# Kernel optimization log

Hardware: AMD Instinct MI355X
Metric: run time of the kernel (lower is better)

The kernel has to match this reference:

```python
import jax, jax.numpy as jnp
import numpy as np

B, S, HID = 2, 2048, 4096
NH, NKV, HD = 32, 8, 128
N_REP = NH // NKV
SCALING = HD ** -0.5


def rotate_half(x):
    x1, x2 = x[..., : x.shape[-1] // 2], x[..., x.shape[-1] // 2 :]
    return jnp.concatenate((-x2, x1), axis=-1)


def setup_inputs() -> dict:
    key = jax.random.key(0)
    ks = jax.random.split(key, 8)
    hidden_states = jax.random.normal(ks[0], (B, S, HID), dtype=jnp.float32)
    # rotary embeddings (realistic cos/sin from inverse-frequency angles)
    inv_freq = 1.0 / (10000.0 ** (jnp.arange(0, HD, 2, dtype=jnp.float32) / HD))
    pos = jnp.arange(S, dtype=jnp.float32)
    ang = pos[:, None] * inv_freq[None, :]  # [S, HD/2]
    emb = jnp.concatenate([ang, ang], axis=-1)  # [S, HD]
    cos = jnp.broadcast_to(jnp.cos(emb)[None], (B, S, HD))
    sin = jnp.broadcast_to(jnp.sin(emb)[None], (B, S, HD))
    # additive causal mask [B,1,S,S]
    causal = jnp.triu(jnp.full((S, S), -1e9, dtype=jnp.float32), k=1)
    attention_mask = jnp.broadcast_to(causal[None, None], (B, 1, S, S))
    std = HID ** -0.5
    Wq = jax.random.normal(ks[1], (NH * HD, HID), dtype=jnp.float32) * std
    Wk = jax.random.normal(ks[2], (NKV * HD, HID), dtype=jnp.float32) * std
    Wv = jax.random.normal(ks[3], (NKV * HD, HID), dtype=jnp.float32) * std
    Wo = jax.random.normal(ks[4], (HID, NH * HD), dtype=jnp.float32) * std
    return {"hidden_states": hidden_states, "cos": cos, "sin": sin,
            "attention_mask": attention_mask, "Wq": Wq, "Wk": Wk, "Wv": Wv, "Wo": Wo}


def reference(hidden_states, cos, sin, attention_mask, Wq, Wk, Wv, Wo):
    b, s, _ = hidden_states.shape
    # projections (nn.Linear: x @ W.T), reshape to [B, H, S, D]
    q = (hidden_states @ Wq.T).reshape(b, s, NH, HD).transpose(0, 2, 1, 3)
    k = (hidden_states @ Wk.T).reshape(b, s, NKV, HD).transpose(0, 2, 1, 3)
    v = (hidden_states @ Wv.T).reshape(b, s, NKV, HD).transpose(0, 2, 1, 3)
    # RoPE, cos/sin broadcast over head dim
    c, sn = cos[:, None], sin[:, None]  # [B,1,S,D]
    q = q * c + rotate_half(q) * sn
    k = k * c + rotate_half(k) * sn
    # GQA repeat_kv
    k = jnp.repeat(k, N_REP, axis=1)
    v = jnp.repeat(v, N_REP, axis=1)
    # eager attention
    attn = jnp.einsum("bhqd,bhkd->bhqk", q, k) * SCALING
    attn = attn + attention_mask[:, :, :, : k.shape[2]]
    attn = jax.nn.softmax(attn.astype(jnp.float32), axis=-1).astype(q.dtype)
    out = jnp.einsum("bhqk,bhkd->bhqd", attn, v)
    out = out.transpose(0, 2, 1, 3).reshape(b, s, NH * HD)
    return out @ Wo.T
```

## Files before the change

kernel.cpp:

```cpp
#include <hip/hip_runtime.h>


typedef __bf16 bf16x8 __attribute__((ext_vector_type(8)));
typedef __bf16 bf16x4 __attribute__((ext_vector_type(4)));
typedef float floatx4 __attribute__((ext_vector_type(4)));

#define S_LEN 2048
#define HIDN  4096
#define NH    32
#define NKV   8
#define HD    128

__device__ inline void async_copy16(const void* g, void* l) {
  __builtin_amdgcn_global_load_lds(
      (const __attribute__((address_space(1))) void*)g,
      (__attribute__((address_space(3))) void*)l, 16, 0, 0);
}

template<int N> __device__ __forceinline__ void waitv() {
  static_assert(N == 0 || N == 6 || N == 8, "vmcnt");
  if constexpr (N == 0)      asm volatile("s_waitcnt vmcnt(0)" ::: "memory");
  else if constexpr (N == 6) asm volatile("s_waitcnt vmcnt(6)" ::: "memory");
  else                       asm volatile("s_waitcnt vmcnt(8)" ::: "memory");
}

__global__ __launch_bounds__(256) void cvt_bf16(const float* __restrict__ src,
                                                __bf16* __restrict__ dst, int n8)
{
  int i = blockIdx.x * 256 + threadIdx.x;
  if (i >= n8) return;
  const float4* s = (const float4*)src + (size_t)i * 2;
  float4 a = s[0], b = s[1];
  bf16x8 r = {(__bf16)a.x, (__bf16)a.y, (__bf16)a.z, (__bf16)a.w,
              (__bf16)b.x, (__bf16)b.y, (__bf16)b.z, (__bf16)b.w};
  *((bf16x8*)dst + i) = r;
}

__device__ __forceinline__ void gemm_core64(
    const __bf16* __restrict__ A, const __bf16* __restrict__ WB,
    __bf16* lds, int m0, int n0, int tid, floatx4 (&acc)[4][4])
{
  constexpr int A_BYTES = 128 * 64 * 2;
  constexpr int STAGE_B = (128 + 256) * 64 * 2;

  const int wave = tid >> 6, lane = tid & 63;
  const int quad = lane >> 4, l16 = lane & 15;
  const int wm = wave >> 2, wn = wave & 3;

  int a_off[2], b_off[4];
  #pragma unroll
  for (int ra = 0; ra < 2; ra++) {
    int idx = ra * 512 + tid;
    int row = idx >> 3, chunk = (idx & 7) ^ (row & 7);
    a_off[ra] = (m0 + row) * HIDN + chunk * 8;
  }
  #pragma unroll
  for (int rb = 0; rb < 4; rb++) {
    int idx = rb * 512 + tid;
    int row = idx >> 3, chunk = (idx & 7) ^ (row & 7);
    b_off[rb] = (n0 + row) * HIDN + chunk * 8;
  }

  const int swq  = (quad ^ (l16 & 3)) * 16;
  const int kxor = ((l16 >> 2) & 1) * 64;
  const int a_rd = (wm * 64 + l16) * 128 + swq;
  const int b_rd = A_BYTES + (wn * 64 + l16) * 128 + swq;

  #pragma unroll
  for (int mi = 0; mi < 4; mi++)
    #pragma unroll
    for (int ni = 0; ni < 4; ni++) acc[mi][ni] = (floatx4){0.f, 0.f, 0.f, 0.f};

  char* ldsb = (char*)lds;
  auto stage = [&](int kt, int slotB) {
    char* sb = ldsb + slotB;
    const size_t ko = (size_t)kt * 64;
    #pragma unroll
    for (int ra = 0; ra < 2; ra++)
      async_copy16(A + ko + a_off[ra], sb + (ra * 512 + tid) * 16);
    #pragma unroll
    for (int rb = 0; rb < 4; rb++)
      async_copy16(WB + ko + b_off[rb], sb + A_BYTES + (rb * 512 + tid) * 16);
  };
  auto read_frags = [&](int slotB, bf16x8 (&av)[4][2], bf16x8 (&bv)[4][2]) {
    const char* sb = ldsb + slotB;
    #pragma unroll
    for (int kk = 0; kk < 2; kk++) {
      const int kb = (kk << 6) ^ kxor;
      #pragma unroll
      for (int ni = 0; ni < 4; ni++)
        bv[ni][kk] = *(const bf16x8*)(sb + b_rd + ni * 2048 + kb);
      #pragma unroll
      for (int mi = 0; mi < 4; mi++)
        av[mi][kk] = *(const bf16x8*)(sb + a_rd + mi * 2048 + kb);
    }
  };
  auto mfma_tile = [&](bf16x8 (&av)[4][2], bf16x8 (&bv)[4][2]) {
    __builtin_amdgcn_s_setprio(1);
    #pragma unroll
    for (int kk = 0; kk < 2; kk++)
      #pragma unroll
      for (int mi = 0; mi < 4; mi++)
        #pragma unroll
        for (int ni = 0; ni < 4; ni++)
          acc[mi][ni] = __builtin_amdgcn_mfma_f32_16x16x32_bf16(
              bv[ni][kk], av[mi][kk], acc[mi][ni], 0, 0, 0);
    __builtin_amdgcn_s_setprio(0);
  };

  bf16x8 avA[4][2], bvA[4][2], avB[4][2], bvB[4][2];

  stage(0, 0);
  stage(1, STAGE_B);
  waitv<6>();
  __builtin_amdgcn_s_barrier();
  asm volatile("" ::: "memory");
  read_frags(0, avA, bvA);

  int oRead = STAGE_B, oStage = 2 * STAGE_B, oFree = 0;

#define GBODY(KT, AVc, BVc, AVn, BVn)                          \
  {                                                            \
    stage((KT) + 2, oStage);                                   \
    waitv<6>();                                                \
    asm volatile("s_waitcnt lgkmcnt(0)" ::: "memory");         \
    __builtin_amdgcn_s_barrier();                              \
    asm volatile("" ::: "memory");                             \
    read_frags(oRead, AVn, BVn);                               \
    mfma_tile(AVc, BVc);                                       \
    int t_ = oFree; oFree = oRead; oRead = oStage; oStage = t_;\
  }

  for (int kt = 0; kt < 62; kt += 2) {
    GBODY(kt,     avA, bvA, avB, bvB);
    GBODY(kt + 1, avB, bvB, avA, bvA);
  }
  {
    waitv<0>();
    asm volatile("s_waitcnt lgkmcnt(0)" ::: "memory");
    __builtin_amdgcn_s_barrier();
    asm volatile("" ::: "memory");
    read_frags(oRead, avB, bvB);
    mfma_tile(avA, bvA);
  }
  mfma_tile(avB, bvB);
#undef GBODY
}

__global__ __launch_bounds__(512, 2) void qkv_gemm_bf16(
    const __bf16* __restrict__ A, const __bf16* __restrict__ WB,
    __bf16* __restrict__ Qb, __bf16* __restrict__ Kb, __bf16* __restrict__ Vt)
{
  __shared__ __bf16 lds[3 * (128 + 256) * 32 * 2];
  const int tid = threadIdx.x;
  const int m0 = blockIdx.y * 128, n0 = blockIdx.x * 256;
  floatx4 acc[4][4];
  gemm_core64(A, WB, lds, m0, n0, tid, acc);

  const int wave = tid >> 6, lane = tid & 63;
  const int quad = lane >> 4, l16 = lane & 15;
  const int wm = wave >> 2, wn = wave & 3;
  #pragma unroll
  for (int mi = 0; mi < 4; mi++) {
    int m = m0 + wm * 64 + mi * 16 + l16;
    int b = m >> 11, s = m & (S_LEN - 1);
    #pragma unroll
    for (int ni = 0; ni < 4; ni++) {
      int nb = n0 + wn * 64 + ni * 16 + quad * 4;
      if (nb < 4096) {
        int hh = nb >> 7, d = nb & 127;
        bf16x4 v = {(__bf16)acc[mi][ni][0], (__bf16)acc[mi][ni][1],
                    (__bf16)acc[mi][ni][2], (__bf16)acc[mi][ni][3]};
        *(bf16x4*)&Qb[(((size_t)b * NH + hh) * S_LEN + s) * HD + d] = v;
      } else if (nb < 5120) {
        int nl = nb - 4096, hh = nl >> 7, d = nl & 127;
        bf16x4 v = {(__bf16)acc[mi][ni][0], (__bf16)acc[mi][ni][1],
                    (__bf16)acc[mi][ni][2], (__bf16)acc[mi][ni][3]};
        *(bf16x4*)&Kb[(((size_t)b * NKV + hh) * S_LEN + s) * HD + d] = v;
      } else {
        int nl = nb - 5120, hh = nl >> 7, d = nl & 127;
        #pragma unroll
        for (int r = 0; r < 4; r++)
          Vt[(((size_t)b * NKV + hh) * HD + d + r) * S_LEN + s] =
              (__bf16)acc[mi][ni][r];
      }
    }
  }
}

__global__ __launch_bounds__(512, 2) void out_gemm_bf16(
    const __bf16* __restrict__ A, const __bf16* __restrict__ WB,
    float* __restrict__ C)
{
  __shared__ __bf16 lds[3 * (128 + 256) * 32 * 2];
  const int tid = threadIdx.x;
  const int m0 = blockIdx.y * 128, n0 = blockIdx.x * 256;
  floatx4 acc[4][4];
  gemm_core64(A, WB, lds, m0, n0, tid, acc);

  const int wave = tid >> 6, lane = tid & 63;
  const int quad = lane >> 4, l16 = lane & 15;
  const int wm = wave >> 2, wn = wave & 3;
  #pragma unroll
  for (int mi = 0; mi < 4; mi++) {
    int m = m0 + wm * 64 + mi * 16 + l16;
    #pragma unroll
    for (int ni = 0; ni < 4; ni++) {
      int nb = n0 + wn * 64 + ni * 16 + quad * 4;
      *(floatx4*)&C[(size_t)m * HIDN + nb] = acc[mi][ni];
    }
  }
}

__global__ __launch_bounds__(256) void qkv_gemm_f32(
    const float* __restrict__ A, const float* __restrict__ Wq,
    const float* __restrict__ Wk, const float* __restrict__ Wv,
    __bf16* __restrict__ Qb, __bf16* __restrict__ Kb, __bf16* __restrict__ Vt)
{
  __shared__ __bf16 As[128 * 40];
  __shared__ __bf16 Bs[128 * 40];
  const int tid  = threadIdx.x;
  const int wave = tid >> 6, lane = tid & 63;
  const int quad = lane >> 4, l16 = lane & 15;
  const int wrow = (wave >> 1) * 64, wcol = (wave & 1) * 64;
  const int m0 = blockIdx.y * 128;
  const int n0 = blockIdx.x * 128;

  const float* W; int wr0; int sel;
  if (n0 < 4096)      { W = Wq; wr0 = n0;        sel = 0; }
  else if (n0 < 5120) { W = Wk; wr0 = n0 - 4096; sel = 1; }
  else                { W = Wv; wr0 = n0 - 5120; sel = 2; }

  floatx4 acc[4][4];
  #pragma unroll
  for (int i = 0; i < 4; i++)
    #pragma unroll
    for (int j = 0; j < 4; j++) acc[i][j] = (floatx4){0.f, 0.f, 0.f, 0.f};

  for (int k0 = 0; k0 < HIDN; k0 += 32) {
    __syncthreads();
    #pragma unroll
    for (int it = 0; it < 4; ++it) {
      int c = tid + it * 256;
      int row = c >> 3, c4 = (c & 7) * 4;
      float4 va = *(const float4*)(A + (size_t)(m0 + row) * HIDN + k0 + c4);
      __bf16* da = &As[row * 40 + c4];
      da[0] = (__bf16)va.x; da[1] = (__bf16)va.y; da[2] = (__bf16)va.z; da[3] = (__bf16)va.w;
      float4 vb = *(const float4*)(W + (size_t)(wr0 + row) * HIDN + k0 + c4);
      __bf16* db = &Bs[row * 40 + c4];
      db[0] = (__bf16)vb.x; db[1] = (__bf16)vb.y; db[2] = (__bf16)vb.z; db[3] = (__bf16)vb.w;
    }
    __syncthreads();
    bf16x8 af[4], bfr[4];
    #pragma unroll
    for (int i = 0; i < 4; i++)
      af[i] = *(const bf16x8*)&As[(wrow + i * 16 + l16) * 40 + quad * 8];
    #pragma unroll
    for (int j = 0; j < 4; j++)
      bfr[j] = *(const bf16x8*)&Bs[(wcol + j * 16 + l16) * 40 + quad * 8];
    #pragma unroll
    for (int i = 0; i < 4; i++)
      #pragma unroll
      for (int j = 0; j < 4; j++)
        acc[i][j] = __builtin_amdgcn_mfma_f32_16x16x32_bf16(af[i], bfr[j], acc[i][j], 0, 0, 0);
  }

  #pragma unroll
  for (int i = 0; i < 4; i++) {
    #pragma unroll
    for (int j = 0; j < 4; j++) {
      #pragma unroll
      for (int r = 0; r < 4; r++) {
        int m = m0 + wrow + i * 16 + quad * 4 + r;
        int n = n0 + wcol + j * 16 + l16;
        __bf16 v = (__bf16)acc[i][j][r];
        int b = m >> 11, s = m & (S_LEN - 1);
        if (sel == 0) {
          int h = n >> 7, d = n & 127;
          Qb[(((size_t)b * NH + h) * S_LEN + s) * HD + d] = v;
        } else if (sel == 1) {
          int nl = n - 4096, h = nl >> 7, d = nl & 127;
          Kb[(((size_t)b * NKV + h) * S_LEN + s) * HD + d] = v;
        } else {
          int nl = n - 5120, h = nl >> 7, d = nl & 127;
          Vt[(((size_t)b * NKV + h) * HD + d) * S_LEN + s] = v;
        }
      }
    }
  }
}

__global__ __launch_bounds__(256) void out_gemm_f32(
    const __bf16* __restrict__ A, const float* __restrict__ Wo,
    float* __restrict__ C)
{
  __shared__ __bf16 As[128 * 40];
  __shared__ __bf16 Bs[128 * 40];
  const int tid  = threadIdx.x;
  const int wave = tid >> 6, lane = tid & 63;
  const int quad = lane >> 4, l16 = lane & 15;
  const int wrow = (wave >> 1) * 64, wcol = (wave & 1) * 64;
  const int m0 = blockIdx.y * 128;
  const int n0 = blockIdx.x * 128;

  floatx4 acc[4][4];
  #pragma unroll
  for (int i = 0; i < 4; i++)
    #pragma unroll
    for (int j = 0; j < 4; j++) acc[i][j] = (floatx4){0.f, 0.f, 0.f, 0.f};

  for (int k0 = 0; k0 < HIDN; k0 += 32) {
    __syncthreads();
    #pragma unroll
    for (int it = 0; it < 2; ++it) {
      int c = tid + it * 256;
      int row = c >> 2, c8 = (c & 3) * 8;
      *(bf16x8*)&As[row * 40 + c8] =
          *(const bf16x8*)(A + (size_t)(m0 + row) * HIDN + k0 + c8);
    }
    #pragma unroll
    for (int it = 0; it < 4; ++it) {
      int c = tid + it * 256;
      int row = c >> 3, c4 = (c & 7) * 4;
      float4 vb = *(const float4*)(Wo + (size_t)(n0 + row) * HIDN + k0 + c4);
      __bf16* db = &Bs[row * 40 + c4];
      db[0] = (__bf16)vb.x; db[1] = (__bf16)vb.y; db[2] = (__bf16)vb.z; db[3] = (__bf16)vb.w;
    }
    __syncthreads();
    bf16x8 af[4], bfr[4];
    #pragma unroll
    for (int i = 0; i < 4; i++)
      af[i] = *(const bf16x8*)&As[(wrow + i * 16 + l16) * 40 + quad * 8];
    #pragma unroll
    for (int j = 0; j < 4; j++)
      bfr[j] = *(const bf16x8*)&Bs[(wcol + j * 16 + l16) * 40 + quad * 8];
    #pragma unroll
    for (int i = 0; i < 4; i++)
      #pragma unroll
      for (int j = 0; j < 4; j++)
        acc[i][j] = __builtin_amdgcn_mfma_f32_16x16x32_bf16(af[i], bfr[j], acc[i][j], 0, 0, 0);
  }

  #pragma unroll
  for (int i = 0; i < 4; i++)
    #pragma unroll
    for (int j = 0; j < 4; j++)
      #pragma unroll
      for (int r = 0; r < 4; r++) {
        int m = m0 + wrow + i * 16 + quad * 4 + r;
        int n = n0 + wcol + j * 16 + l16;
        C[(size_t)m * HIDN + n] = acc[i][j][r];
      }
}

__global__ __launch_bounds__(256) void rope_kernel(
    __bf16* __restrict__ Qb, __bf16* __restrict__ Kb,
    const float* __restrict__ cosp, const float* __restrict__ sinp)
{
  size_t i = (size_t)blockIdx.x * 256 + threadIdx.x;
  const size_t QP = (size_t)2 * NH * S_LEN * 8;
  __bf16* buf; int H; size_t t;
  if (i < QP) { buf = Qb; H = NH;  t = i; }
  else        { buf = Kb; H = NKV; t = i - QP; }
  int d0 = (int)(t & 7) * 8;
  int s  = (int)((t >> 3) & (S_LEN - 1));
  size_t rest = t >> 14;
  int h = (int)(rest % H);
  int b = (int)(rest / H);
  size_t base = (((size_t)b * H + h) * S_LEN + s) * HD;
  bf16x8 q0 = *(const bf16x8*)&buf[base + d0];
  bf16x8 q1 = *(const bf16x8*)&buf[base + d0 + 64];
  size_t cbase = ((size_t)b * S_LEN + s) * HD + d0;
  float4 c0 = *(const float4*)&cosp[cbase];
  float4 c1 = *(const float4*)&cosp[cbase + 4];
  float4 s0 = *(const float4*)&sinp[cbase];
  float4 s1 = *(const float4*)&sinp[cbase + 4];
  float cc[8] = {c0.x, c0.y, c0.z, c0.w, c1.x, c1.y, c1.z, c1.w};
  float ss[8] = {s0.x, s0.y, s0.z, s0.w, s1.x, s1.y, s1.z, s1.w};
  bf16x8 r0, r1;
  #pragma unroll
  for (int u = 0; u < 8; u++) {
    float a  = (float)q0[u];
    float bq = (float)q1[u];
    r0[u] = (__bf16)(a * cc[u] - bq * ss[u]);
    r1[u] = (__bf16)(bq * cc[u] + a * ss[u]);
  }
  *(bf16x8*)&buf[base + d0]      = r0;
  *(bf16x8*)&buf[base + d0 + 64] = r1;
}

__global__ __launch_bounds__(256, 2) void flash_attn(
    const __bf16* __restrict__ Q, const __bf16* __restrict__ Kc,
    const __bf16* __restrict__ Vt, __bf16* __restrict__ Out)
{
  __shared__ __bf16 Ks2[2][64 * 128];
  __shared__ __bf16 VTs2[2][128 * 64];
  __shared__ __bf16 Ps[4 * 32 * 64];
  const int tid  = threadIdx.x;
  const int wave = tid >> 6, lane = tid & 63;
  const int quad = lane >> 4, l16 = lane & 15;
  const int bh = blockIdx.x;
  const int h = bh & 31, b = bh >> 5;
  const int qt = 15 - (int)blockIdx.y;
  const int kvh = h >> 2;
  const size_t qbase  = (((size_t)b * NH + h) * S_LEN + qt * 128 + wave * 32) * HD;
  const size_t kbase  = ((size_t)b * NKV + kvh) * S_LEN * HD;
  const size_t vtbase = ((size_t)b * NKV + kvh) * (size_t)HD * S_LEN;
  const int psbase = wave * (32 * 64);

  int ksrc[4], vsrc[4];
  #pragma unroll
  for (int it = 0; it < 4; ++it) {
    int idx = it * 256 + tid;
    { int r = idx >> 4, cs = idx & 15, cg = cs ^ (r & 15);
      ksrc[it] = r * HD + cg * 8; }
    { int r = idx >> 3, cs = idx & 7, cg = cs ^ (r & 7);
      vsrc[it] = r * S_LEN + cg * 8; }
  }
  auto stageKV = [&](int kj, int slot) {
    const __bf16* kp = Kc + kbase + (size_t)kj * 64 * HD;
    const __bf16* vp = Vt + vtbase + (size_t)kj * 64;
    char* kd = (char*)&Ks2[slot][0];
    char* vd = (char*)&VTs2[slot][0];
    #pragma unroll
    for (int it = 0; it < 4; ++it) {
      int dst = (it * 256 + tid) * 16;
      async_copy16(kp + ksrc[it], kd + dst);
      async_copy16(vp + vsrc[it], vd + dst);
    }
  };

  bf16x8 qf[2][4];
  #pragma unroll
  for (int st = 0; st < 2; st++)
    #pragma unroll
    for (int kk = 0; kk < 4; kk++)
      qf[st][kk] = *(const bf16x8*)&Q[qbase + (size_t)(st * 16 + l16) * HD + kk * 32 + quad * 8];

  floatx4 o[2][8];
  floatx4 ol[2];
  #pragma unroll
  for (int st = 0; st < 2; st++) {
    ol[st] = (floatx4){0.f, 0.f, 0.f, 0.f};
    #pragma unroll
    for (int ct = 0; ct < 8; ct++) o[st][ct] = (floatx4){0.f, 0.f, 0.f, 0.f};
  }
  bf16x8 onesv;
  #pragma unroll
  for (int u = 0; u < 8; u++) onesv[u] = (__bf16)1.0f;

  const float c1 = 0.12753785f;
  const float c2 = -28.853900f;
  const int kj_end = 2 * qt + 2;

  stageKV(0, 0);
  stageKV(1, 1);

  for (int kj = 0; kj < kj_end; ++kj) {
    const int slot = kj & 1;
    if (kj == 0) waitv<8>();
    else         waitv<0>();
    asm volatile("s_waitcnt lgkmcnt(0)" ::: "memory");
    __builtin_amdgcn_s_barrier();
    asm volatile("" ::: "memory");
    if (kj >= 1 && kj + 1 < kj_end) stageKV(kj + 1, (kj + 1) & 1);

    const __bf16* Ksl = &Ks2[slot][0];
    const __bf16* Vsl = &VTs2[slot][0];

    floatx4 s[2][4];
    #pragma unroll
    for (int st = 0; st < 2; st++)
      #pragma unroll
      for (int j = 0; j < 4; j++) s[st][j] = (floatx4){0.f, 0.f, 0.f, 0.f};
    #pragma unroll
    for (int kk = 0; kk < 4; kk++) {
      bf16x8 ak[4];
      #pragma unroll
      for (int j = 0; j < 4; j++)
        ak[j] = *(const bf16x8*)&Ksl[(j * 16 + l16) * 128 + (((kk * 4 + quad) ^ l16) * 8)];
      __builtin_amdgcn_s_setprio(1);
      #pragma unroll
      for (int st = 0; st < 2; st++)
        #pragma unroll
        for (int j = 0; j < 4; j++)
          s[st][j] = __builtin_amdgcn_mfma_f32_16x16x32_bf16(ak[j], qf[st][kk], s[st][j], 0, 0, 0);
      __builtin_amdgcn_s_setprio(0);
    }

    #pragma unroll
    for (int st = 0; st < 2; st++) {
      const int qrow = qt * 128 + wave * 32 + st * 16 + l16;
      #pragma unroll
      for (int j = 0; j < 4; j++) {
        const int kvb = kj * 64 + j * 16 + quad * 4;
        bf16x4 pw;
        #pragma unroll
        for (int r = 0; r < 4; r++) {
          float p = __builtin_amdgcn_exp2f(fmaf(s[st][j][r], c1, c2));
          if (kvb + r > qrow) p = 0.0f;
          pw[r] = (__bf16)p;
        }
        *(bf16x4*)&Ps[psbase + (st * 16 + l16) * 64 + (((j * 4 + quad) ^ (l16 & 14)) * 4)] = pw;
      }
    }

    #pragma unroll
    for (int kk = 0; kk < 2; kk++) {
      bf16x8 bv[8];
      #pragma unroll
      for (int ct = 0; ct < 8; ct++)
        bv[ct] = *(const bf16x8*)&Vsl[(ct * 16 + l16) * 64 + (((kk * 4 + quad) ^ (l16 & 7)) * 8)];
      bf16x8 ap[2];
      #pragma unroll
      for (int st = 0; st < 2; st++)
        ap[st] = *(const bf16x8*)&Ps[psbase + (st * 16 + l16) * 64 + (((kk * 8 + quad * 2) ^ (l16 & 14)) * 4)];
      __builtin_amdgcn_s_setprio(1);
      #pragma unroll
      for (int st = 0; st < 2; st++) {
        ol[st] = __builtin_amdgcn_mfma_f32_16x16x32_bf16(ap[st], onesv, ol[st], 0, 0, 0);
        #pragma unroll
        for (int ct = 0; ct < 8; ct++)
          o[st][ct] = __builtin_amdgcn_mfma_f32_16x16x32_bf16(ap[st], bv[ct], o[st][ct], 0, 0, 0);
      }
      __builtin_amdgcn_s_setprio(0);
    }
  }

  #pragma unroll
  for (int st = 0; st < 2; st++) {
    #pragma unroll
    for (int r = 0; r < 4; r++) {
      float rl = 1.0f / ol[st][r];
      int qi = qt * 128 + wave * 32 + st * 16 + quad * 4 + r;
      #pragma unroll
      for (int ct = 0; ct < 8; ct++) {
        Out[((size_t)b * S_LEN + qi) * HIDN + h * HD + ct * 16 + l16] =
            (__bf16)(o[st][ct][r] * rl);
      }
    }
  }
}

extern "C" void kernel_launch(void* const* d_in, const int* in_sizes, int n_in,
                              void* d_out, int out_size, void* d_ws, size_t ws_size,
                              hipStream_t stream)
{
  const float* hs   = (const float*)d_in[0];
  const float* cosp = (const float*)d_in[1];
  const float* sinp = (const float*)d_in[2];
  const float* Wq   = (const float*)d_in[4];
  const float* Wk   = (const float*)d_in[5];
  const float* Wv   = (const float*)d_in[6];
  const float* Wo   = (const float*)d_in[7];
  float* out = (float*)d_out;

  __bf16* Qb  = (__bf16*)d_ws;
  __bf16* Kb  = Qb  + (size_t)16777216;
  __bf16* Vtb = Kb  + (size_t)4194304;

  if (ws_size >= (size_t)134217728) {
    __bf16* HSB = Vtb + (size_t)4194304;
    __bf16* AO  = HSB;
    __bf16* WB  = HSB + (size_t)16777216;

    cvt_bf16<<<8192, 256, 0, stream>>>(hs, HSB, 2097152);
    cvt_bf16<<<8192, 256, 0, stream>>>(Wq, WB, 2097152);
    cvt_bf16<<<2048, 256, 0, stream>>>(Wk, WB + 16777216, 524288);
    cvt_bf16<<<2048, 256, 0, stream>>>(Wv, WB + 20971520, 524288);
    qkv_gemm_bf16<<<dim3(24, 32), 512, 0, stream>>>(HSB, WB, Qb, Kb, Vtb);
    cvt_bf16<<<8192, 256, 0, stream>>>(Wo, WB, 2097152);
    rope_kernel<<<5120, 256, 0, stream>>>(Qb, Kb, cosp, sinp);
    flash_attn<<<dim3(64, 16), 256, 0, stream>>>(Qb, Kb, Vtb, AO);
    out_gemm_bf16<<<dim3(16, 32), 512, 0, stream>>>(AO, WB, out);
  } else {
    __bf16* AO = Vtb + (size_t)4194304;
    qkv_gemm_f32<<<dim3(48, 32), 256, 0, stream>>>(hs, Wq, Wk, Wv, Qb, Kb, Vtb);
    rope_kernel<<<5120, 256, 0, stream>>>(Qb, Kb, cosp, sinp);
    flash_attn<<<dim3(64, 16), 256, 0, stream>>>(Qb, Kb, Vtb, AO);
    out_gemm_f32<<<dim3(32, 32), 256, 0, stream>>>(AO, Wo, out);
  }
}
```

Measured before the change: 666.9 us.

## Load GEMM B operand directly from global into registers, bypassing LDS

The shared GEMM core now stages only the A tile through LDS and loads B (weight) fragments straight from global memory into registers, one k-step ahead. LDS use drops to a third, and the B LDS writes and reads disappear. In exchange, each wave issues uncoalesced 16-byte global loads with no reuse across the two M-waves sharing B columns. The pipeline now waits on vmcnt(0) every iteration, which exposes global latency and shortens prefetch depth.

```diff
diff --git a/kernel.cpp b/kernel.cpp
--- a/kernel.cpp
+++ b/kernel.cpp
@@ -18,10 +18,9 @@
 }
 
 template<int N> __device__ __forceinline__ void waitv() {
-  static_assert(N == 0 || N == 6 || N == 8, "vmcnt");
-  if constexpr (N == 0)      asm volatile("s_waitcnt vmcnt(0)" ::: "memory");
-  else if constexpr (N == 6) asm volatile("s_waitcnt vmcnt(6)" ::: "memory");
-  else                       asm volatile("s_waitcnt vmcnt(8)" ::: "memory");
+  static_assert(N == 0 || N == 8, "vmcnt");
+  if constexpr (N == 0) asm volatile("s_waitcnt vmcnt(0)" ::: "memory");
+  else                  asm volatile("s_waitcnt vmcnt(8)" ::: "memory");
 }
 
 __global__ __launch_bounds__(256) void cvt_bf16(const float* __restrict__ src,
@@ -40,31 +39,25 @@
     const __bf16* __restrict__ A, const __bf16* __restrict__ WB,
     __bf16* lds, int m0, int n0, int tid, floatx4 (&acc)[4][4])
 {
-  constexpr int A_BYTES = 128 * 64 * 2;
-  constexpr int STAGE_B = (128 + 256) * 64 * 2;
+  constexpr int ASTG = 128 * 64 * 2;
 
   const int wave = tid >> 6, lane = tid & 63;
   const int quad = lane >> 4, l16 = lane & 15;
   const int wm = wave >> 2, wn = wave & 3;
 
-  int a_off[2], b_off[4];
+  int a_off[2];
   #pragma unroll
   for (int ra = 0; ra < 2; ra++) {
     int idx = ra * 512 + tid;
     int row = idx >> 3, chunk = (idx & 7) ^ (row & 7);
     a_off[ra] = (m0 + row) * HIDN + chunk * 8;
   }
-  #pragma unroll
-  for (int rb = 0; rb < 4; rb++) {
-    int idx = rb * 512 + tid;
-    int row = idx >> 3, chunk = (idx & 7) ^ (row & 7);
-    b_off[rb] = (n0 + row) * HIDN + chunk * 8;
-  }
 
   const int swq  = (quad ^ (l16 & 3)) * 16;
   const int kxor = ((l16 >> 2) & 1) * 64;
   const int a_rd = (wm * 64 + l16) * 128 + swq;
-  const int b_rd = A_BYTES + (wn * 64 + l16) * 128 + swq;
+
+  const __bf16* bbase = WB + (size_t)(n0 + wn * 64 + l16) * HIDN + quad * 8;
 
   #pragma unroll
   for (int mi = 0; mi < 4; mi++)
@@ -72,24 +65,25 @@
     for (int ni = 0; ni < 4; ni++) acc[mi][ni] = (floatx4){0.f, 0.f, 0.f, 0.f};
 
   char* ldsb = (char*)lds;
-  auto stage = [&](int kt, int slotB) {
+  auto stageA = [&](int kt, int slotB) {
     char* sb = ldsb + slotB;
     const size_t ko = (size_t)kt * 64;
     #pragma unroll
     for (int ra = 0; ra < 2; ra++)
       async_copy16(A + ko + a_off[ra], sb + (ra * 512 + tid) * 16);
-    #pragma unroll
-    for (int rb = 0; rb < 4; rb++)
-      async_copy16(WB + ko + b_off[rb], sb + A_BYTES + (rb * 512 + tid) * 16);
   };
-  auto read_frags = [&](int slotB, bf16x8 (&av)[4][2], bf16x8 (&bv)[4][2]) {
+  auto loadB = [&](int kt, bf16x8 (&bv)[4][2]) {
+    #pragma unroll
+    for (int ni = 0; ni < 4; ni++)
+      #pragma unroll
+      for (int kk = 0; kk < 2; kk++)
+        bv[ni][kk] = *(const bf16x8*)(bbase + (size_t)ni * (16 * HIDN) + kt * 64 + kk * 32);
+  };
+  auto readA = [&](int slotB, bf16x8 (&av)[4][2]) {
     const char* sb = ldsb + slotB;
     #pragma unroll
     for (int kk = 0; kk < 2; kk++) {
       const int kb = (kk << 6) ^ kxor;
-      #pragma unroll
-      for (int ni = 0; ni < 4; ni++)
-        bv[ni][kk] = *(const bf16x8*)(sb + b_rd + ni * 2048 + kb);
       #pragma unroll
       for (int mi = 0; mi < 4; mi++)
         av[mi][kk] = *(const bf16x8*)(sb + a_rd + mi * 2048 + kb);
@@ -110,23 +104,28 @@
 
   bf16x8 avA[4][2], bvA[4][2], avB[4][2], bvB[4][2];
 
-  stage(0, 0);
-  stage(1, STAGE_B);
-  waitv<6>();
+  stageA(0, 0);
+  stageA(1, ASTG);
+  asm volatile("" ::: "memory");
+  loadB(0, bvA);
+  asm volatile("" ::: "memory");
+  asm volatile("s_waitcnt vmcnt(10)" ::: "memory");
   __builtin_amdgcn_s_barrier();
   asm volatile("" ::: "memory");
-  read_frags(0, avA, bvA);
-
-  int oRead = STAGE_B, oStage = 2 * STAGE_B, oFree = 0;
+  readA(0, avA);
+
+  int oRead = ASTG, oStage = 2 * ASTG, oFree = 0;
 
 #define GBODY(KT, AVc, BVc, AVn, BVn)                          \
   {                                                            \
-    stage((KT) + 2, oStage);                                   \
-    waitv<6>();                                                \
+    asm volatile("s_waitcnt vmcnt(0)" ::: "memory");           \
     asm volatile("s_waitcnt lgkmcnt(0)" ::: "memory");         \
     __builtin_amdgcn_s_barrier();                              \
     asm volatile("" ::: "memory");                             \
-    read_frags(oRead, AVn, BVn);                               \
+    loadB((KT) + 1, BVn);                                      \
+    stageA((KT) + 2, oStage);                                  \
+    asm volatile("" ::: "memory");                             \
+    readA(oRead, AVn);                                         \
     mfma_tile(AVc, BVc);                                       \
     int t_ = oFree; oFree = oRead; oRead = oStage; oStage = t_;\
   }
@@ -136,14 +135,20 @@
     GBODY(kt + 1, avB, bvB, avA, bvA);
   }
   {
-    waitv<0>();
+    asm volatile("s_waitcnt vmcnt(0)" ::: "memory");
     asm volatile("s_waitcnt lgkmcnt(0)" ::: "memory");
     __builtin_amdgcn_s_barrier();
     asm volatile("" ::: "memory");
-    read_frags(oRead, avB, bvB);
+    loadB(63, bvB);
+    asm volatile("" ::: "memory");
+    readA(oRead, avB);
     mfma_tile(avA, bvA);
   }
-  mfma_tile(avB, bvB);
+  {
+    asm volatile("s_waitcnt vmcnt(0)" ::: "memory");
+    asm volatile("s_waitcnt lgkmcnt(0)" ::: "memory");
+    mfma_tile(avB, bvB);
+  }
 #undef GBODY
 }
 
@@ -151,7 +156,7 @@
     const __bf16* __restrict__ A, const __bf16* __restrict__ WB,
     __bf16* __restrict__ Qb, __bf16* __restrict__ Kb, __bf16* __restrict__ Vt)
 {
-  __shared__ __bf16 lds[3 * (128 + 256) * 32 * 2];
+  __shared__ __bf16 lds[3 * 128 * 64];
   const int tid = threadIdx.x;
   const int m0 = blockIdx.y * 128, n0 = blockIdx.x * 256;
   floatx4 acc[4][4];
@@ -192,7 +197,7 @@
     const __bf16* __restrict__ A, const __bf16* __restrict__ WB,
     float* __restrict__ C)
 {
-  __shared__ __bf16 lds[3 * (128 + 256) * 32 * 2];
+  __shared__ __bf16 lds[3 * 128 * 64];
   const int tid = threadIdx.x;
   const int m0 = blockIdx.y * 128, n0 = blockIdx.x * 256;
   floatx4 acc[4][4];
```

Result: slower. 1.089 ms (+63.3%).
